# Kernel optimization log

Hardware: AMD Instinct MI355X
Metric: run time of the kernel (lower is better)

The kernel has to match this reference:

```python
import jax, jax.numpy as jnp
from jax import lax
import numpy as np

LOGZERO = -1e10  # matches the repo's `logzero` sentinel


def setup_inputs() -> dict:
    key = jax.random.key(0)
    k1, k2, k3, k4 = jax.random.split(key, 4)
    bs, xmax, vocab, ymax = 32, 1024, 1000, 128
    # CTC log-probabilities (ctc_generator output is log_softmax in the repo)
    ctc_out = jax.nn.log_softmax(
        jax.random.normal(k1, (bs, xmax, vocab), jnp.float32), axis=-1)
    src_size = jax.random.randint(k2, (bs,), xmax // 2, xmax + 1)
    src_mask = (jnp.arange(xmax)[None, :] < src_size[:, None])[:, None, :]  # [bs,1,xmax] bool
    ys = jax.random.randint(k3, (bs, ymax), 1, vocab)   # non-blank labels
    ylens = jax.random.randint(k4, (bs,), ymax // 2, ymax + 1)
    return {"ctc_out": ctc_out, "src_mask": src_mask, "src_size": src_size,
            "ys": ys, "ylens": ylens, "blank": 0}


def reference(ctc_out, src_mask, src_size, ys, ylens, blank):
    bs, xmax, vocab = ctc_out.shape
    ymax = ys.shape[1]
    L = 2 * ymax + 1  # blank-interleaved path length

    # mask invalid frames to logzero (masked_fill in torch)
    lp = jnp.where(src_mask.transpose(0, 2, 1), ctc_out, LOGZERO)  # [bs,xmax,vocab]

    # blank-interleaved path: [blank, y1, blank, y2, ..., blank]
    path = jnp.full((bs, L), blank, dtype=ys.dtype).at[:, 1::2].set(ys)
    path_lens = 2 * ylens + 1

    # log-probs gathered along the path: [xmax, bs, L] (time-major for scan)
    lp_path = jnp.take_along_axis(
        lp, jnp.broadcast_to(path[:, None, :], (bs, xmax, L)), axis=2)
    lp_path = lp_path.transpose(1, 0, 2)

    same_tr = path[:, :-2] == path[:, 2:]                 # [bs, L-2]
    idx = jnp.arange(L)
    outside = idx[None, :] >= path_lens[:, None]          # [bs, L]

    alpha0 = jnp.full((bs, L), LOGZERO, jnp.float32).at[:, 0].set(0.0)

    def step(alpha, lp_t):
        m0 = alpha
        m1 = jnp.concatenate([jnp.full((bs, 1), LOGZERO, alpha.dtype), alpha[:, :-1]], axis=1)
        m2 = jnp.concatenate([jnp.full((bs, 2), LOGZERO, alpha.dtype),
                              jnp.where(same_tr, LOGZERO, alpha[:, :-2])], axis=1)
        mat = jnp.stack([m0, m1, m2])                     # [3, bs, L]
        max_prob = jnp.max(mat, axis=0)
        arg = jnp.argmax(mat, axis=0)
        bp_t = idx[None, :] - arg                          # back-pointer (path position)
        max_prob = jnp.where(outside, LOGZERO, max_prob)
        alpha_new = max_prob + lp_t
        return alpha_new, (alpha_new, bp_t)

    _, (alpha_hist, bp) = lax.scan(step, alpha0, lp_path)  # [xmax,bs,L] each
    alpha_full = jnp.concatenate([alpha0[None], alpha_hist], axis=0)  # [xmax+1,bs,L]

    b_idx = jnp.arange(bs)
    alpha_at = alpha_full[src_size, b_idx]                 # [bs, L] alpha at t = src_size
    s1 = alpha_at[b_idx, path_lens - 1]
    s2 = alpha_at[b_idx, path_lens - 2]
    start = jnp.where(s1 > s2, path_lens - 1, path_lens - 2)
    score = jnp.maximum(s1, s2)                            # best alignment log-prob per utt

    # vectorized backtrace over all batches (reverse scan over time)
    def back_step(carry, t):
        tt = jnp.minimum(t + 1, xmax - 1)
        prev = bp[tt, b_idx, carry]                        # bp[b, t+1, state_{t+1}]
        val = jnp.where(t == src_size - 1, start,
                        jnp.where(t < src_size - 1, prev, 0))
        return val, val

    ts = jnp.arange(xmax - 1, -1, -1)
    _, states_rev = lax.scan(back_step, jnp.zeros((bs,), start.dtype), ts)
    states = states_rev[::-1].T                            # [bs, xmax] path positions

    aligned = jnp.take_along_axis(path, states, axis=1)    # [bs, xmax] tokens
    shift = jnp.concatenate([jnp.zeros((bs, 1), aligned.dtype), aligned[:, :-1]], axis=1)
    aligned = jnp.where(aligned == shift, 0, aligned)      # collapse repeats to 0
    shift2 = jnp.concatenate([jnp.zeros((bs, 1), aligned.dtype), aligned[:, :-1]], axis=1)

    csum = jnp.cumsum((shift2 != blank).astype(jnp.int32), axis=1)  # [bs, xmax]
    tm = csum[:, None, :] == jnp.arange(ymax + 1)[None, :, None]    # [bs, ymax+1, xmax]
    last = tm[:, -1, :] & src_mask[:, 0, :]
    last = last.at[b_idx, src_size - 1].set(True)
    tm = tm.at[:, -1, :].set(last)
    trigger_mask = tm & src_mask                           # & x_mask from FaNat.forward

    return score, trigger_mask, ylens + 1
```

## Files before the change

### kernel.cpp

```cpp
#include <hip/hip_runtime.h>
#include <stdint.h>

#define LOGZERO (-1e10f)

static constexpr int BS    = 32;
static constexpr int XMAX  = 1024;
static constexpr int VOCAB = 1000;
static constexpr int YMAX  = 128;
static constexpr int NROWS = YMAX + 1;
static constexpr int CH    = 8;
static constexpr int NPROD = 8;
static constexpr int NWAVES = 1 + NPROD;
static constexpr int NPAIR = XMAX / 2;
static constexpr size_t LPWS_BYTES = (size_t)BS * XMAX * 256 * 4;

__device__ __forceinline__ float rot1(float x) {
    int r = __builtin_amdgcn_update_dpp(0, __float_as_int(x),
                                        0x13C , 0xF, 0xF, false);
    return __int_as_float(r);
}

__global__ __launch_bounds__(256) void k_gather(
    const float* __restrict__ ctc, const int* __restrict__ src_size,
    const int* __restrict__ ys, const int* __restrict__ blankp,
    float* __restrict__ lp_ws)
{
    const int blk  = blockIdx.x;
    const int b    = blk >> 4;
    const int seg  = blk & 15;
    const int wid  = threadIdx.x >> 6;
    const int lane = threadIdx.x & 63;
    const int ss   = src_size[b];
    const int bv   = blankp[0];
    const int tokA = ys[b * YMAX + 2 * lane];
    const int tokB = ys[b * YMAX + 2 * lane + 1];
    const float* baseg = ctc + (size_t)b * XMAX * VOCAB;
    float* basew = lp_ws + (size_t)b * XMAX * 256 + lane * 4;
    const int t0 = seg * 64 + wid * 16;
    #pragma unroll 4
    for (int r = 0; r < 16; ++r) {
        const int t = t0 + r;
        if (t < ss) {
            const float* rp = baseg + (size_t)t * VOCAB;
            float vb = rp[bv], va = rp[tokA], vc = rp[tokB];
            *reinterpret_cast<float4*>(basew + (size_t)t * 256) =
                make_float4(vb, va, vb, vc);
        }
    }
}

#define VSTEP(qq, PK, SHIFT, RBIT) do {                                     \
    float rot = rot1(a3);                       \
    float p3  = (lane == 0) ? LZ : rot;                                     \
    float sk1 = al1 ? p3 : LZ;                                              \
    float sk3 = al3 ? a1 : LZ;                                              \
    float m0 = fmaxf(a0, p3);                                               \
    float m1 = fmaxf(fmaxf(a1, a0), sk1);                                   \
    float m2 = fmaxf(a2, a1);                                               \
    float m3 = fmaxf(fmaxf(a3, a2), sk3);                                   \
    unsigned gb = (a0 == m0 ? 0u : 1u)                                      \
                | (a1 == m1 ? 0u : (a0 == m1 ? 4u : 8u))                    \
                | (a2 == m2 ? 0u : 16u)                                     \
                | (a3 == m3 ? 0u : (a2 == m3 ? 64u : 128u));                \
    if (W4) {                                                               \
        float m4 = fmaxf(a4, rot);                                          \
        g4acc |= (a4 == m4 ? 0u : 1u) << (RBIT);                            \
        a4 = m4 + (qq).x;                       \
    }                                                                       \
    a0 = m0 + (qq).x; a1 = m1 + (qq).y; a2 = m2 + (qq).z; a3 = m3 + (qq).w; \
    PK |= gb << (SHIFT);                                                    \
} while (0)

template<bool W4>
__device__ __forceinline__ void viterbi_loop(
    int lane, int ss, bool al1, bool al3, float LZ,
    float (&buf)[2][CH][256], unsigned int* bpb32, unsigned char* g4pack,
    float& a0, float& a1, float& a2, float& a3, float& a4)
{
    const int nfull = ss >> 3;
    const int mrem  = ss & 7;
    for (int c = 0; c < nfull; ++c) {
        __builtin_amdgcn_s_barrier();
        asm volatile("" ::: "memory");
        __builtin_amdgcn_sched_barrier(0);
        const int cb = c & 1;
        float4 q[CH];
        #pragma unroll
        for (int r = 0; r < CH; ++r)
            q[r] = *reinterpret_cast<const float4*>(&buf[cb][r][lane * 4]);
        unsigned int pkA = 0, pkB = 0, g4acc = 0;
        #pragma unroll
        for (int r = 0; r < 4; ++r) VSTEP(q[r], pkA, r * 8, r);
        #pragma unroll
        for (int r = 4; r < 8; ++r) VSTEP(q[r], pkB, (r - 4) * 8, r);
        bpb32[(2 * c) * 64 + lane]     = pkA;
        bpb32[(2 * c + 1) * 64 + lane] = pkB;
        if (W4) { if (lane == 0) g4pack[c] = (unsigned char)g4acc; }
    }
    if (mrem) {
        __builtin_amdgcn_s_barrier();
        asm volatile("" ::: "memory");
        __builtin_amdgcn_sched_barrier(0);
        const int cb = nfull & 1;
        float4 q[CH];
        #pragma unroll
        for (int r = 0; r < CH; ++r)
            q[r] = *reinterpret_cast<const float4*>(&buf[cb][r][lane * 4]);
        unsigned int pkA = 0, pkB = 0, g4acc = 0;
        #pragma unroll
        for (int r = 0; r < 4; ++r)
            if (r < mrem) VSTEP(q[r], pkA, r * 8, r);
        #pragma unroll
        for (int r = 4; r < 8; ++r)
            if (r < mrem) VSTEP(q[r], pkB, (r - 4) * 8, r);
        bpb32[(2 * nfull) * 64 + lane] = pkA;
        if (mrem > 4) bpb32[(2 * nfull + 1) * 64 + lane] = pkB;
        if (W4) { if (lane == 0) g4pack[nfull] = (unsigned char)g4acc; }
    }
}

template<bool STAGED>
__global__ __launch_bounds__(64 * NWAVES) void k_viterbi(
    const float* __restrict__ ctc, const float* __restrict__ lp_ws,
    const int* __restrict__ src_size,
    const int* __restrict__ ys, const int* __restrict__ ylens,
    const int* __restrict__ blankp, int* __restrict__ csum_ws,
    float* __restrict__ out)
{
    __shared__ float buf[2][CH][256];
    __shared__ unsigned int  bpb32[(XMAX / 4) * 64];
    __shared__ unsigned char  g4pack[XMAX / CH];
    __shared__ unsigned short bp2[NPAIR * 64];
    __shared__ unsigned char  bp2_256[NPAIR];
    __shared__ unsigned short st_lds[XMAX];
    __shared__ int ysl[YMAX];

    const int b    = blockIdx.x;
    const int tid  = threadIdx.x;
    const int wid  = tid >> 6;
    const int lane = tid & 63;
    const int ss   = src_size[b];
    const int yl   = ylens[b];
    const int bv   = blankp[0];
    const int plen = 2 * yl + 1;
    const float LZ = LOGZERO;

    for (int j = tid; j < YMAX; j += 64 * NWAVES) ysl[j] = ys[b * YMAX + j];
    for (int t = tid; t < XMAX; t += 64 * NWAVES) st_lds[t] = 0;
    __syncthreads();

    const int nchunk = (ss + CH - 1) / CH;
    const float* baseg = ctc + (size_t)b * XMAX * VOCAB;

    int start = 0;

    if (wid == 0) {
        const int tokA = ysl[2 * lane];
        const int tokB = ysl[2 * lane + 1];
        const bool al1 = (lane > 0) && (tokA != ysl[2 * lane - 1]);
        const bool al3 = (tokB != tokA);

        float a0 = (lane == 0) ? 0.0f : LZ;
        float a1 = LZ, a2 = LZ, a3 = LZ, a4 = LZ;

        if (plen > 256)
            viterbi_loop<true >(lane, ss, al1, al3, LZ, buf, bpb32, g4pack,
                                a0, a1, a2, a3, a4);
        else
            viterbi_loop<false>(lane, ss, al1, al3, LZ, buf, bpb32, g4pack,
                                a0, a1, a2, a3, a4);

        auto getA = [&](int idx) -> float {
            if (idx == 256) return __shfl(a4, 0);
            int k = idx & 3;
            float pick = (k == 0) ? a0 : (k == 1) ? a1 : (k == 2) ? a2 : a3;
            return __shfl(pick, idx >> 2);
        };
        const float s1v = getA(plen - 1), s2v = getA(plen - 2);
        const float score = (s1v > s2v) ? s1v : s2v;
        start = (s1v > s2v) ? (plen - 1) : (plen - 2);
        if (lane == 0) {
            out[b] = score;
            out[32 + (size_t)BS * NROWS * XMAX + b] = (float)(yl + 1);
        }
    } else if (STAGED) {
        const int pr = wid - 1;
        const float* basew = lp_ws + (size_t)b * XMAX * 256 + lane * 4;
        auto ldrow = [&](int cc) -> float4 {
            int tn = cc * CH + pr; if (tn > XMAX - 1) tn = XMAX - 1;
            return *reinterpret_cast<const float4*>(basew + (size_t)tn * 256);
        };
        float4 v0 = ldrow(0), v1 = ldrow(1), v2 = ldrow(2), v3 = ldrow(3);
        int c = 0;
        for (;;) {
            *reinterpret_cast<float4*>(&buf[c & 1][pr][lane * 4]) = v0;
            v0 = ldrow(c + 4);
            asm volatile("s_waitcnt lgkmcnt(0)" ::: "memory");
            __builtin_amdgcn_s_barrier();
            if (++c >= nchunk) break;
            *reinterpret_cast<float4*>(&buf[c & 1][pr][lane * 4]) = v1;
            v1 = ldrow(c + 4);
            asm volatile("s_waitcnt lgkmcnt(0)" ::: "memory");
            __builtin_amdgcn_s_barrier();
            if (++c >= nchunk) break;
            *reinterpret_cast<float4*>(&buf[c & 1][pr][lane * 4]) = v2;
            v2 = ldrow(c + 4);
            asm volatile("s_waitcnt lgkmcnt(0)" ::: "memory");
            __builtin_amdgcn_s_barrier();
            if (++c >= nchunk) break;
            *reinterpret_cast<float4*>(&buf[c & 1][pr][lane * 4]) = v3;
            v3 = ldrow(c + 4);
            asm volatile("s_waitcnt lgkmcnt(0)" ::: "memory");
            __builtin_amdgcn_s_barrier();
            if (++c >= nchunk) break;
        }
    } else {
        const int pr = wid - 1;
        const int tokA = ysl[2 * lane];
        const int tokB = ysl[2 * lane + 1];
        int t0 = pr; if (t0 >= ss) t0 = ss - 1;
        const float* r0 = baseg + (size_t)t0 * VOCAB;
        float vb0 = r0[bv], va0 = r0[tokA], vc0 = r0[tokB];
        int t1 = CH + pr; if (t1 >= ss) t1 = ss - 1;
        const float* r1 = baseg + (size_t)t1 * VOCAB;
        float vb1 = r1[bv], va1 = r1[tokA], vc1 = r1[tokB];
        for (int c = 0; c < nchunk; ++c) {
            if (c & 1) {
                *reinterpret_cast<float4*>(&buf[1][pr][lane * 4]) =
                    make_float4(vb1, va1, vb1, vc1);
                int tn = (c + 2) * CH + pr; if (tn >= ss) tn = ss - 1;
                const float* r = baseg + (size_t)tn * VOCAB;
                vb1 = r[bv]; va1 = r[tokA]; vc1 = r[tokB];
            } else {
                *reinterpret_cast<float4*>(&buf[0][pr][lane * 4]) =
                    make_float4(vb0, va0, vb0, vc0);
                int tn = (c + 2) * CH + pr; if (tn >= ss) tn = ss - 1;
                const float* r = baseg + (size_t)tn * VOCAB;
                vb0 = r[bv]; va0 = r[tokA]; vc0 = r[tokB];
            }
            asm volatile("s_waitcnt lgkmcnt(0)" ::: "memory");
            __builtin_amdgcn_s_barrier();
        }
    }
    __syncthreads();

    const unsigned char* bpb8 = reinterpret_cast<const unsigned char*>(bpb32);
    #define BPBYTE(t, l) ((int)bpb8[(((t) >> 2) * 64 + (l)) * 4 + ((t) & 3)])

    const int pmax = (ss - 1) >> 1;
    for (int p = 1 + wid; p <= pmax; p += NWAVES) {
        int oOdd  = BPBYTE(2 * p + 1, lane);
        int oEven = BPBYTE(2 * p, lane);
        int uEven = (lane > 0) ? BPBYTE(2 * p, lane - 1) : 0;
        int evenWin = uEven | (oEven << 8);
        unsigned int acc = 0;
        #pragma unroll
        for (int k = 0; k < 4; ++k) {
            int a1v = (oOdd >> (2 * k)) & 3;
            int sh  = 2 * k - 2 * a1v + 8;
            int a2v = (evenWin >> sh) & 3;
            acc |= (unsigned)(a1v | (a2v << 2)) << (4 * k);
        }
        bp2[p * 64 + lane] = (unsigned short)acc;
        const int tOdd = 2 * p + 1, tEven = 2 * p;
        int a16 = (g4pack[tOdd >> 3] >> (tOdd & 7)) & 1;
        int a26 = (a16 == 0) ? ((g4pack[tEven >> 3] >> (tEven & 7)) & 1)
                             : ((BPBYTE(tEven, 63) >> 6) & 3);
        if (lane == 0) bp2_256[p] = (unsigned char)(a16 | (a26 << 2));
    }
    __syncthreads();

    if (tid == 0) {
        int s = start, tc = ss - 1;
        st_lds[tc] = (unsigned short)s;
        if ((tc & 1) == 0 && tc >= 1) {
            int arg;
            if (s == 256) arg = (g4pack[tc >> 3] >> (tc & 7)) & 1;
            else arg = (BPBYTE(tc, s >> 2) >> ((s & 3) * 2)) & 3;
            s -= arg; --tc; st_lds[tc] = (unsigned short)s;
        }
        while (tc > 1) {
            int n;
            if (s == 256) n = bp2_256[tc >> 1];
            else n = (bp2[(tc >> 1) * 64 + (s >> 2)] >> ((s & 3) * 4)) & 0xF;
            int sA = s - (n & 3);
            int sB = sA - (n >> 2);
            st_lds[tc - 1] = (unsigned short)sA;
            st_lds[tc - 2] = (unsigned short)sB;
            s = sB; tc -= 2;
        }
        if (tc == 1) {
            int arg;
            if (s == 256) arg = (g4pack[0] >> 1) & 1;
            else arg = (BPBYTE(1, s >> 2) >> ((s & 3) * 2)) & 3;
            s -= arg; st_lds[0] = (unsigned short)s;
        }
    }
    #undef BPBYTE
    __syncthreads();

    if (wid == 0) {
        auto tok_lds = [&](int stv) -> int { return (stv & 1) ? ysl[stv >> 1] : bv; };
        const int t0c = lane * 16;
        int prev_raw = (t0c == 0) ? 0 : tok_lds(st_lds[t0c - 1]);
        int cnt = 0;
        int csl[16];
        #pragma unroll
        for (int i = 0; i < 16; ++i) {
            int raw = tok_lds(st_lds[t0c + i]);
            int ac = (raw == prev_raw) ? 0 : raw;
            prev_raw = raw;
            csl[i] = cnt;
            cnt += (ac != bv) ? 1 : 0;
        }
        int v = cnt;
        #pragma unroll
        for (int off = 1; off < 64; off <<= 1) {
            int u = __shfl_up(v, off);
            if (lane >= off) v += u;
        }
        const int base_c = v - cnt;
        int* co = csum_ws + b * XMAX + t0c;
        #pragma unroll
        for (int i = 0; i < 16; ++i) co[i] = base_c + csl[i];
    }
}

__global__ __launch_bounds__(256) void k_mask(
    const int* __restrict__ csum_ws, const int* __restrict__ src_size,
    float* __restrict__ out)
{
    int bj = blockIdx.x;
    int b = bj / NROWS, j = bj - b * NROWS;
    int ss = src_size[b];
    const int* cs = csum_ws + b * XMAX;
    float* orow = out + 32 + (size_t)bj * XMAX;
    int t = threadIdx.x * 4;
    float4 v;
    float* vp = &v.x;
    #pragma unroll
    for (int i = 0; i < 4; ++i) {
        int tt = t + i;
        int c = cs[tt];
        bool in = tt < ss;
        bool val;
        if (j < YMAX) val = (c == j) && in;
        else          val = ((c == YMAX) || (tt == ss - 1)) && in;
        vp[i] = val ? 1.0f : 0.0f;
    }
    *(float4*)(orow + t) = v;
}

extern "C" void kernel_launch(void* const* d_in, const int* in_sizes, int n_in,
                              void* d_out, int out_size, void* d_ws, size_t ws_size,
                              hipStream_t stream) {
    const float* ctc      = (const float*)d_in[0];
    const int*   src_size = (const int*)d_in[2];
    const int*   ys       = (const int*)d_in[3];
    const int*   ylens    = (const int*)d_in[4];
    const int*   blankp   = (const int*)d_in[5];
    float* out = (float*)d_out;

    const size_t need = LPWS_BYTES + (size_t)BS * XMAX * sizeof(int);
    if (ws_size >= need) {
        float* lp_ws   = (float*)d_ws;
        int*   csum_ws = (int*)((char*)d_ws + LPWS_BYTES);
        k_gather<<<BS * 16, 256, 0, stream>>>(ctc, src_size, ys, blankp, lp_ws);
        k_viterbi<true><<<BS, 64 * NWAVES, 0, stream>>>(
            ctc, lp_ws, src_size, ys, ylens, blankp, csum_ws, out);
        k_mask<<<BS * NROWS, 256, 0, stream>>>(csum_ws, src_size, out);
    } else {
        int* csum_ws = (int*)d_ws;
        k_viterbi<false><<<BS, 64 * NWAVES, 0, stream>>>(
            ctc, nullptr, src_size, ys, ylens, blankp, csum_ws, out);
        k_mask<<<BS * NROWS, 256, 0, stream>>>(csum_ws, src_size, out);
    }
}
```

Before: 340.3 us.

## Stream staged log-probs into LDS via direct global-to-LDS loads in Viterbi wave

In the staged path, the Viterbi wave now fetches its own chunks from the gathered workspace using global_load_lds, which writes straight into a triple-buffered LDS ring. This replaces the eight producer waves and their per-chunk block barriers. Synchronisation drops to vmcnt/lgkmcnt waits inside one wave, removing barrier latency from the serial recurrence. The cost is a larger LDS buffer and reliance on the async-load counter accounting, with three chunks kept in flight. The producer waves still launch but sit idle in the staged path.

```diff
diff --git a/kernel.cpp b/kernel.cpp
--- a/kernel.cpp
+++ b/kernel.cpp
@@ -18,6 +18,12 @@
     int r = __builtin_amdgcn_update_dpp(0, __float_as_int(x),
                                         0x13C , 0xF, 0xF, false);
     return __int_as_float(r);
+}
+
+__device__ __forceinline__ void gload16(const float* g, float* l) {
+    __builtin_amdgcn_global_load_lds(
+        (const __attribute__((address_space(1))) void*)g,
+        (__attribute__((address_space(3))) void*)l, 16, 0, 0);
 }
 
 __global__ __launch_bounds__(256) void k_gather(
@@ -72,9 +78,70 @@
 } while (0)
 
 template<bool W4>
-__device__ __forceinline__ void viterbi_loop(
+__device__ __forceinline__ void viterbi_loop_staged(
     int lane, int ss, bool al1, bool al3, float LZ,
-    float (&buf)[2][CH][256], unsigned int* bpb32, unsigned char* g4pack,
+    float (&buf)[3][CH][256], unsigned int* bpb32, unsigned char* g4pack,
+    const float* basew,
+    float& a0, float& a1, float& a2, float& a3, float& a4)
+{
+    const int nfull = ss >> 3;
+    const int mrem  = ss & 7;
+
+    auto issue_chunk = [&](int cc, int cb) {
+        int ccl = cc; if (ccl > XMAX / CH - 1) ccl = XMAX / CH - 1;
+        const float* g0 = basew + (size_t)ccl * (CH * 256);
+        #pragma unroll
+        for (int r = 0; r < CH; ++r)
+            gload16(g0 + r * 256, &buf[cb][r][0]);
+    };
+    issue_chunk(0, 0); issue_chunk(1, 1); issue_chunk(2, 2);
+
+    int cb = 0;
+    for (int c = 0; c < nfull; ++c) {
+        asm volatile("s_waitcnt vmcnt(16)" ::: "memory");
+        __builtin_amdgcn_sched_barrier(0);
+        float4 q[CH];
+        #pragma unroll
+        for (int r = 0; r < CH; ++r)
+            q[r] = *reinterpret_cast<const float4*>(&buf[cb][r][lane * 4]);
+        asm volatile("s_waitcnt lgkmcnt(0)" ::: "memory");
+        __builtin_amdgcn_sched_barrier(0);
+        issue_chunk(c + 3, cb);
+        __builtin_amdgcn_sched_barrier(0);
+        unsigned int pkA = 0, pkB = 0, g4acc = 0;
+        #pragma unroll
+        for (int r = 0; r < 4; ++r) VSTEP(q[r], pkA, r * 8, r);
+        #pragma unroll
+        for (int r = 4; r < 8; ++r) VSTEP(q[r], pkB, (r - 4) * 8, r);
+        bpb32[(2 * c) * 64 + lane]     = pkA;
+        bpb32[(2 * c + 1) * 64 + lane] = pkB;
+        if (W4) { if (lane == 0) g4pack[c] = (unsigned char)g4acc; }
+        cb = (cb == 2) ? 0 : cb + 1;
+    }
+    if (mrem) {
+        asm volatile("s_waitcnt vmcnt(16)" ::: "memory");
+        __builtin_amdgcn_sched_barrier(0);
+        float4 q[CH];
+        #pragma unroll
+        for (int r = 0; r < CH; ++r)
+            q[r] = *reinterpret_cast<const float4*>(&buf[cb][r][lane * 4]);
+        unsigned int pkA = 0, pkB = 0, g4acc = 0;
+        #pragma unroll
+        for (int r = 0; r < 4; ++r)
+            if (r < mrem) VSTEP(q[r], pkA, r * 8, r);
+        #pragma unroll
+        for (int r = 4; r < 8; ++r)
+            if (r < mrem) VSTEP(q[r], pkB, (r - 4) * 8, r);
+        bpb32[(2 * nfull) * 64 + lane] = pkA;
+        if (mrem > 4) bpb32[(2 * nfull + 1) * 64 + lane] = pkB;
+        if (W4) { if (lane == 0) g4pack[nfull] = (unsigned char)g4acc; }
+    }
+}
+
+template<bool W4>
+__device__ __forceinline__ void viterbi_loop_ring(
+    int lane, int ss, bool al1, bool al3, float LZ,
+    float (&buf)[3][CH][256], unsigned int* bpb32, unsigned char* g4pack,
     float& a0, float& a1, float& a2, float& a3, float& a4)
 {
     const int nfull = ss >> 3;
@@ -127,7 +194,7 @@
     const int* __restrict__ blankp, int* __restrict__ csum_ws,
     float* __restrict__ out)
 {
-    __shared__ float buf[2][CH][256];
+    __shared__ float buf[3][CH][256];
     __shared__ unsigned int  bpb32[(XMAX / 4) * 64];
     __shared__ unsigned char  g4pack[XMAX / CH];
     __shared__ unsigned short bp2[NPAIR * 64];
@@ -163,12 +230,22 @@
         float a0 = (lane == 0) ? 0.0f : LZ;
         float a1 = LZ, a2 = LZ, a3 = LZ, a4 = LZ;
 
-        if (plen > 256)
-            viterbi_loop<true >(lane, ss, al1, al3, LZ, buf, bpb32, g4pack,
-                                a0, a1, a2, a3, a4);
-        else
-            viterbi_loop<false>(lane, ss, al1, al3, LZ, buf, bpb32, g4pack,
-                                a0, a1, a2, a3, a4);
+        if (STAGED) {
+            const float* basew = lp_ws + (size_t)b * XMAX * 256 + lane * 4;
+            if (plen > 256)
+                viterbi_loop_staged<true >(lane, ss, al1, al3, LZ, buf, bpb32,
+                                           g4pack, basew, a0, a1, a2, a3, a4);
+            else
+                viterbi_loop_staged<false>(lane, ss, al1, al3, LZ, buf, bpb32,
+                                           g4pack, basew, a0, a1, a2, a3, a4);
+        } else {
+            if (plen > 256)
+                viterbi_loop_ring<true >(lane, ss, al1, al3, LZ, buf, bpb32,
+                                         g4pack, a0, a1, a2, a3, a4);
+            else
+                viterbi_loop_ring<false>(lane, ss, al1, al3, LZ, buf, bpb32,
+                                         g4pack, a0, a1, a2, a3, a4);
+        }
 
         auto getA = [&](int idx) -> float {
             if (idx == 256) return __shfl(a4, 0);
@@ -183,38 +260,7 @@
             out[b] = score;
             out[32 + (size_t)BS * NROWS * XMAX + b] = (float)(yl + 1);
         }
-    } else if (STAGED) {
-        const int pr = wid - 1;
-        const float* basew = lp_ws + (size_t)b * XMAX * 256 + lane * 4;
-        auto ldrow = [&](int cc) -> float4 {
-            int tn = cc * CH + pr; if (tn > XMAX - 1) tn = XMAX - 1;
-            return *reinterpret_cast<const float4*>(basew + (size_t)tn * 256);
-        };
-        float4 v0 = ldrow(0), v1 = ldrow(1), v2 = ldrow(2), v3 = ldrow(3);
-        int c = 0;
-        for (;;) {
-            *reinterpret_cast<float4*>(&buf[c & 1][pr][lane * 4]) = v0;
-            v0 = ldrow(c + 4);
-            asm volatile("s_waitcnt lgkmcnt(0)" ::: "memory");
-            __builtin_amdgcn_s_barrier();
-            if (++c >= nchunk) break;
-            *reinterpret_cast<float4*>(&buf[c & 1][pr][lane * 4]) = v1;
-            v1 = ldrow(c + 4);
-            asm volatile("s_waitcnt lgkmcnt(0)" ::: "memory");
-            __builtin_amdgcn_s_barrier();
-            if (++c >= nchunk) break;
-            *reinterpret_cast<float4*>(&buf[c & 1][pr][lane * 4]) = v2;
-            v2 = ldrow(c + 4);
-            asm volatile("s_waitcnt lgkmcnt(0)" ::: "memory");
-            __builtin_amdgcn_s_barrier();
-            if (++c >= nchunk) break;
-            *reinterpret_cast<float4*>(&buf[c & 1][pr][lane * 4]) = v3;
-            v3 = ldrow(c + 4);
-            asm volatile("s_waitcnt lgkmcnt(0)" ::: "memory");
-            __builtin_amdgcn_s_barrier();
-            if (++c >= nchunk) break;
-        }
-    } else {
+    } else if (!STAGED) {
         const int pr = wid - 1;
         const int tokA = ysl[2 * lane];
         const int tokB = ysl[2 * lane + 1];
```

Measured after the change: 349.1 us. +2.6%, slower.

## Fuse gather, Viterbi and mask into one kernel with per-segment flag sync

Applied to the files above, without the earlier changes.

Merges the separate gather, Viterbi and mask kernels into one launch. Extra blocks gather the path log-probs into the workspace and publish per-segment release flags. The Viterbi producer waves spin on those flags so decoding can begin before the whole gather finishes. The cumsum and trigger-mask output are also computed inside the Viterbi block, which drops the csum workspace round trip and two launches. The cost is a memset plus spin-wait synchronisation, which relies on the Viterbi blocks (lowest IDs) being scheduled alongside the gather blocks, and the mask writes now come from only 32 blocks.

```diff
diff --git a/kernel.cpp b/kernel.cpp
--- a/kernel.cpp
+++ b/kernel.cpp
@@ -12,41 +12,14 @@
 static constexpr int NPROD = 8;
 static constexpr int NWAVES = 1 + NPROD;
 static constexpr int NPAIR = XMAX / 2;
+static constexpr int NSEG  = 16;
 static constexpr size_t LPWS_BYTES = (size_t)BS * XMAX * 256 * 4;
+static constexpr size_t FLAGS_BYTES = (size_t)BS * NSEG * sizeof(int);
 
 __device__ __forceinline__ float rot1(float x) {
     int r = __builtin_amdgcn_update_dpp(0, __float_as_int(x),
                                         0x13C , 0xF, 0xF, false);
     return __int_as_float(r);
-}
-
-__global__ __launch_bounds__(256) void k_gather(
-    const float* __restrict__ ctc, const int* __restrict__ src_size,
-    const int* __restrict__ ys, const int* __restrict__ blankp,
-    float* __restrict__ lp_ws)
-{
-    const int blk  = blockIdx.x;
-    const int b    = blk >> 4;
-    const int seg  = blk & 15;
-    const int wid  = threadIdx.x >> 6;
-    const int lane = threadIdx.x & 63;
-    const int ss   = src_size[b];
-    const int bv   = blankp[0];
-    const int tokA = ys[b * YMAX + 2 * lane];
-    const int tokB = ys[b * YMAX + 2 * lane + 1];
-    const float* baseg = ctc + (size_t)b * XMAX * VOCAB;
-    float* basew = lp_ws + (size_t)b * XMAX * 256 + lane * 4;
-    const int t0 = seg * 64 + wid * 16;
-    #pragma unroll 4
-    for (int r = 0; r < 16; ++r) {
-        const int t = t0 + r;
-        if (t < ss) {
-            const float* rp = baseg + (size_t)t * VOCAB;
-            float vb = rp[bv], va = rp[tokA], vc = rp[tokB];
-            *reinterpret_cast<float4*>(basew + (size_t)t * 256) =
-                make_float4(vb, va, vb, vc);
-        }
-    }
 }
 
 #define VSTEP(qq, PK, SHIFT, RBIT) do {                                     \
@@ -72,7 +45,7 @@
 } while (0)
 
 template<bool W4>
-__device__ __forceinline__ void viterbi_loop(
+__device__ __forceinline__ void viterbi_loop_ring(
     int lane, int ss, bool al1, bool al3, float LZ,
     float (&buf)[2][CH][256], unsigned int* bpb32, unsigned char* g4pack,
     float& a0, float& a1, float& a2, float& a3, float& a4)
@@ -119,13 +92,11 @@
     }
 }
 
-template<bool STAGED>
-__global__ __launch_bounds__(64 * NWAVES) void k_viterbi(
-    const float* __restrict__ ctc, const float* __restrict__ lp_ws,
-    const int* __restrict__ src_size,
+__global__ __launch_bounds__(64 * NWAVES) void k_fused(
+    const float* __restrict__ ctc, float* __restrict__ lp_ws,
+    int* __restrict__ flags, const int* __restrict__ src_size,
     const int* __restrict__ ys, const int* __restrict__ ylens,
-    const int* __restrict__ blankp, int* __restrict__ csum_ws,
-    float* __restrict__ out)
+    const int* __restrict__ blankp, float* __restrict__ out)
 {
     __shared__ float buf[2][CH][256];
     __shared__ unsigned int  bpb32[(XMAX / 4) * 64];
@@ -133,12 +104,42 @@
     __shared__ unsigned short bp2[NPAIR * 64];
     __shared__ unsigned char  bp2_256[NPAIR];
     __shared__ unsigned short st_lds[XMAX];
+    __shared__ int cs_lds[XMAX];
     __shared__ int ysl[YMAX];
 
-    const int b    = blockIdx.x;
     const int tid  = threadIdx.x;
     const int wid  = tid >> 6;
     const int lane = tid & 63;
+
+    if (blockIdx.x >= BS) {
+        const int gidx = blockIdx.x - BS;
+        const int seg  = gidx >> 5;
+        const int b    = gidx & 31;
+        const int ss   = src_size[b];
+        const int bv   = blankp[0];
+        const int tokA = ys[b * YMAX + 2 * lane];
+        const int tokB = ys[b * YMAX + 2 * lane + 1];
+        const float* baseg = ctc + (size_t)b * XMAX * VOCAB;
+        float* basew = lp_ws + (size_t)b * XMAX * 256 + lane * 4;
+        for (int r = wid; r < 64; r += NWAVES) {
+            const int t = seg * 64 + r;
+            if (t < ss) {
+                const float* rp = baseg + (size_t)t * VOCAB;
+                float vb = rp[bv], va = rp[tokA], vc = rp[tokB];
+                *reinterpret_cast<float4*>(basew + (size_t)t * 256) =
+                    make_float4(vb, va, vb, vc);
+            }
+        }
+        __syncthreads();
+        if (tid == 0) {
+            __threadfence();
+            __hip_atomic_store(&flags[b * NSEG + seg], 1,
+                               __ATOMIC_RELEASE, __HIP_MEMORY_SCOPE_AGENT);
+        }
+        return;
+    }
+
+    const int b    = blockIdx.x;
     const int ss   = src_size[b];
     const int yl   = ylens[b];
     const int bv   = blankp[0];
@@ -150,8 +151,6 @@
     __syncthreads();
 
     const int nchunk = (ss + CH - 1) / CH;
-    const float* baseg = ctc + (size_t)b * XMAX * VOCAB;
-
     int start = 0;
 
     if (wid == 0) {
@@ -164,11 +163,11 @@
         float a1 = LZ, a2 = LZ, a3 = LZ, a4 = LZ;
 
         if (plen > 256)
-            viterbi_loop<true >(lane, ss, al1, al3, LZ, buf, bpb32, g4pack,
-                                a0, a1, a2, a3, a4);
+            viterbi_loop_ring<true >(lane, ss, al1, al3, LZ, buf, bpb32,
+                                     g4pack, a0, a1, a2, a3, a4);
         else
-            viterbi_loop<false>(lane, ss, al1, al3, LZ, buf, bpb32, g4pack,
-                                a0, a1, a2, a3, a4);
+            viterbi_loop_ring<false>(lane, ss, al1, al3, LZ, buf, bpb32,
+                                     g4pack, a0, a1, a2, a3, a4);
 
         auto getA = [&](int idx) -> float {
             if (idx == 256) return __shfl(a4, 0);
@@ -183,36 +182,198 @@
             out[b] = score;
             out[32 + (size_t)BS * NROWS * XMAX + b] = (float)(yl + 1);
         }
-    } else if (STAGED) {
+    } else {
         const int pr = wid - 1;
         const float* basew = lp_ws + (size_t)b * XMAX * 256 + lane * 4;
+        int* flg = flags + b * NSEG;
+        auto waitseg = [&](int s) {
+            while (__hip_atomic_load(&flg[s], __ATOMIC_ACQUIRE,
+                                     __HIP_MEMORY_SCOPE_AGENT) == 0)
+                __builtin_amdgcn_s_sleep(2);
+        };
         auto ldrow = [&](int cc) -> float4 {
             int tn = cc * CH + pr; if (tn > XMAX - 1) tn = XMAX - 1;
             return *reinterpret_cast<const float4*>(basew + (size_t)tn * 256);
         };
+        waitseg(0);
         float4 v0 = ldrow(0), v1 = ldrow(1), v2 = ldrow(2), v3 = ldrow(3);
+        int slast = 0;
         int c = 0;
-        for (;;) {
-            *reinterpret_cast<float4*>(&buf[c & 1][pr][lane * 4]) = v0;
-            v0 = ldrow(c + 4);
-            asm volatile("s_waitcnt lgkmcnt(0)" ::: "memory");
-            __builtin_amdgcn_s_barrier();
-            if (++c >= nchunk) break;
-            *reinterpret_cast<float4*>(&buf[c & 1][pr][lane * 4]) = v1;
-            v1 = ldrow(c + 4);
-            asm volatile("s_waitcnt lgkmcnt(0)" ::: "memory");
-            __builtin_amdgcn_s_barrier();
-            if (++c >= nchunk) break;
-            *reinterpret_cast<float4*>(&buf[c & 1][pr][lane * 4]) = v2;
-            v2 = ldrow(c + 4);
-            asm volatile("s_waitcnt lgkmcnt(0)" ::: "memory");
-            __builtin_amdgcn_s_barrier();
-            if (++c >= nchunk) break;
-            *reinterpret_cast<float4*>(&buf[c & 1][pr][lane * 4]) = v3;
-            v3 = ldrow(c + 4);
-            asm volatile("s_waitcnt lgkmcnt(0)" ::: "memory");
-            __builtin_amdgcn_s_barrier();
-            if (++c >= nchunk) break;
+#define PPHASE(VV)                                                          \
+        *reinterpret_cast<float4*>(&buf[c & 1][pr][lane * 4]) = VV;         \
+        { int row = (c + 4) * CH + pr; if (row > XMAX - 1) row = XMAX - 1;  \
+          int sn = row >> 6;                                                \
+          if (sn != slast) { waitseg(sn); slast = sn; } }                   \
+        VV = ldrow(c + 4);                                                  \
+        asm volatile("s_waitcnt lgkmcnt(0)" ::: "memory");                  \
+        __builtin_amdgcn_s_barrier();                                       \
+        if (++c >= nchunk) break;
+        for (;;) { PPHASE(v0) PPHASE(v1) PPHASE(v2) PPHASE(v3) }
+#undef PPHASE
+    }
+    __syncthreads();
+
+    const unsigned char* bpb8 = reinterpret_cast<const unsigned char*>(bpb32);
+    #define BPBYTE(t, l) ((int)bpb8[(((t) >> 2) * 64 + (l)) * 4 + ((t) & 3)])
+
+    const int pmax = (ss - 1) >> 1;
+    for (int p = 1 + wid; p <= pmax; p += NWAVES) {
+        int oOdd  = BPBYTE(2 * p + 1, lane);
+        int oEven = BPBYTE(2 * p, lane);
+        int uEven = (lane > 0) ? BPBYTE(2 * p, lane - 1) : 0;
+        int evenWin = uEven | (oEven << 8);
+        unsigned int acc = 0;
+        #pragma unroll
+        for (int k = 0; k < 4; ++k) {
+            int a1v = (oOdd >> (2 * k)) & 3;
+            int sh  = 2 * k - 2 * a1v + 8;
+            int a2v = (evenWin >> sh) & 3;
+            acc |= (unsigned)(a1v | (a2v << 2)) << (4 * k);
+        }
+        bp2[p * 64 + lane] = (unsigned short)acc;
+        const int tOdd = 2 * p + 1, tEven = 2 * p;
+        int a16 = (g4pack[tOdd >> 3] >> (tOdd & 7)) & 1;
+        int a26 = (a16 == 0) ? ((g4pack[tEven >> 3] >> (tEven & 7)) & 1)
+                             : ((BPBYTE(tEven, 63) >> 6) & 3);
+        if (lane == 0) bp2_256[p] = (unsigned char)(a16 | (a26 << 2));
+    }
+    __syncthreads();
+
+    if (tid == 0) {
+        int s = start, tc = ss - 1;
+        st_lds[tc] = (unsigned short)s;
+        if ((tc & 1) == 0 && tc >= 1) {
+            int arg;
+            if (s == 256) arg = (g4pack[tc >> 3] >> (tc & 7)) & 1;
+            else arg = (BPBYTE(tc, s >> 2) >> ((s & 3) * 2)) & 3;
+            s -= arg; --tc; st_lds[tc] = (unsigned short)s;
+        }
+        while (tc > 1) {
+            int n;
+            if (s == 256) n = bp2_256[tc >> 1];
+            else n = (bp2[(tc >> 1) * 64 + (s >> 2)] >> ((s & 3) * 4)) & 0xF;
+            int sA = s - (n & 3);
+            int sB = sA - (n >> 2);
+            st_lds[tc - 1] = (unsigned short)sA;
+            st_lds[tc - 2] = (unsigned short)sB;
+            s = sB; tc -= 2;
+        }
+        if (tc == 1) {
+            int arg;
+            if (s == 256) arg = (g4pack[0] >> 1) & 1;
+            else arg = (BPBYTE(1, s >> 2) >> ((s & 3) * 2)) & 3;
+            s -= arg; st_lds[0] = (unsigned short)s;
+        }
+    }
+    #undef BPBYTE
+    __syncthreads();
+
+    if (wid == 0) {
+        auto tok_lds = [&](int stv) -> int { return (stv & 1) ? ysl[stv >> 1] : bv; };
+        const int t0c = lane * 16;
+        int prev_raw = (t0c == 0) ? 0 : tok_lds(st_lds[t0c - 1]);
+        int cnt = 0;
+        int csl[16];
+        #pragma unroll
+        for (int i = 0; i < 16; ++i) {
+            int raw = tok_lds(st_lds[t0c + i]);
+            int ac = (raw == prev_raw) ? 0 : raw;
+            prev_raw = raw;
+            csl[i] = cnt;
+            cnt += (ac != bv) ? 1 : 0;
+        }
+        int v = cnt;
+        #pragma unroll
+        for (int off = 1; off < 64; off <<= 1) {
+            int u = __shfl_up(v, off);
+            if (lane >= off) v += u;
+        }
+        const int base_c = v - cnt;
+        #pragma unroll
+        for (int i = 0; i < 16; ++i) cs_lds[t0c + i] = base_c + csl[i];
+    }
+    __syncthreads();
+
+    for (int j = wid; j < NROWS; j += NWAVES) {
+        float* orow = out + 32 + ((size_t)b * NROWS + j) * XMAX;
+        const int t0c = lane * 16;
+        #pragma unroll
+        for (int q4 = 0; q4 < 4; ++q4) {
+            const int t = t0c + q4 * 4;
+            float4 v;
+            float* vp = &v.x;
+            #pragma unroll
+            for (int i = 0; i < 4; ++i) {
+                int tt = t + i;
+                int c = cs_lds[tt];
+                bool in = tt < ss;
+                bool val;
+                if (j < YMAX) val = (c == j) && in;
+                else          val = ((c == YMAX) || (tt == ss - 1)) && in;
+                vp[i] = val ? 1.0f : 0.0f;
+            }
+            *(float4*)(orow + t) = v;
+        }
+    }
+}
+
+__global__ __launch_bounds__(64 * NWAVES) void k_viterbi_fb(
+    const float* __restrict__ ctc, const int* __restrict__ src_size,
+    const int* __restrict__ ys, const int* __restrict__ ylens,
+    const int* __restrict__ blankp, int* __restrict__ csum_ws,
+    float* __restrict__ out)
+{
+    __shared__ float buf[2][CH][256];
+    __shared__ unsigned int  bpb32[(XMAX / 4) * 64];
+    __shared__ unsigned char  g4pack[XMAX / CH];
+    __shared__ unsigned short bp2[NPAIR * 64];
+    __shared__ unsigned char  bp2_256[NPAIR];
+    __shared__ unsigned short st_lds[XMAX];
+    __shared__ int ysl[YMAX];
+
+    const int b    = blockIdx.x;
+    const int tid  = threadIdx.x;
+    const int wid  = tid >> 6;
+    const int lane = tid & 63;
+    const int ss   = src_size[b];
+    const int yl   = ylens[b];
+    const int bv   = blankp[0];
+    const int plen = 2 * yl + 1;
+    const float LZ = LOGZERO;
+
+    for (int j = tid; j < YMAX; j += 64 * NWAVES) ysl[j] = ys[b * YMAX + j];
+    for (int t = tid; t < XMAX; t += 64 * NWAVES) st_lds[t] = 0;
+    __syncthreads();
+
+    const int nchunk = (ss + CH - 1) / CH;
+    const float* baseg = ctc + (size_t)b * XMAX * VOCAB;
+    int start = 0;
+
+    if (wid == 0) {
+        const int tokA = ysl[2 * lane];
+        const int tokB = ysl[2 * lane + 1];
+        const bool al1 = (lane > 0) && (tokA != ysl[2 * lane - 1]);
+        const bool al3 = (tokB != tokA);
+        float a0 = (lane == 0) ? 0.0f : LZ;
+        float a1 = LZ, a2 = LZ, a3 = LZ, a4 = LZ;
+        if (plen > 256)
+            viterbi_loop_ring<true >(lane, ss, al1, al3, LZ, buf, bpb32,
+                                     g4pack, a0, a1, a2, a3, a4);
+        else
+            viterbi_loop_ring<false>(lane, ss, al1, al3, LZ, buf, bpb32,
+                                     g4pack, a0, a1, a2, a3, a4);
+        auto getA = [&](int idx) -> float {
+            if (idx == 256) return __shfl(a4, 0);
+            int k = idx & 3;
+            float pick = (k == 0) ? a0 : (k == 1) ? a1 : (k == 2) ? a2 : a3;
+            return __shfl(pick, idx >> 2);
+        };
+        const float s1v = getA(plen - 1), s2v = getA(plen - 2);
+        const float score = (s1v > s2v) ? s1v : s2v;
+        start = (s1v > s2v) ? (plen - 1) : (plen - 2);
+        if (lane == 0) {
+            out[b] = score;
+            out[32 + (size_t)BS * NROWS * XMAX + b] = (float)(yl + 1);
         }
     } else {
         const int pr = wid - 1;
@@ -246,7 +407,6 @@
 
     const unsigned char* bpb8 = reinterpret_cast<const unsigned char*>(bpb32);
     #define BPBYTE(t, l) ((int)bpb8[(((t) >> 2) * 64 + (l)) * 4 + ((t) & 3)])
-
     const int pmax = (ss - 1) >> 1;
     for (int p = 1 + wid; p <= pmax; p += NWAVES) {
         int oOdd  = BPBYTE(2 * p + 1, lane);
@@ -361,18 +521,17 @@
     const int*   blankp   = (const int*)d_in[5];
     float* out = (float*)d_out;
 
-    const size_t need = LPWS_BYTES + (size_t)BS * XMAX * sizeof(int);
+    const size_t need = LPWS_BYTES + FLAGS_BYTES;
     if (ws_size >= need) {
-        float* lp_ws   = (float*)d_ws;
-        int*   csum_ws = (int*)((char*)d_ws + LPWS_BYTES);
-        k_gather<<<BS * 16, 256, 0, stream>>>(ctc, src_size, ys, blankp, lp_ws);
-        k_viterbi<true><<<BS, 64 * NWAVES, 0, stream>>>(
-            ctc, lp_ws, src_size, ys, ylens, blankp, csum_ws, out);
-        k_mask<<<BS * NROWS, 256, 0, stream>>>(csum_ws, src_size, out);
+        float* lp_ws = (float*)d_ws;
+        int*   flags = (int*)((char*)d_ws + LPWS_BYTES);
+        hipMemsetAsync(flags, 0, FLAGS_BYTES, stream);
+        k_fused<<<BS + BS * NSEG, 64 * NWAVES, 0, stream>>>(
+            ctc, lp_ws, flags, src_size, ys, ylens, blankp, out);
     } else {
         int* csum_ws = (int*)d_ws;
-        k_viterbi<false><<<BS, 64 * NWAVES, 0, stream>>>(
-            ctc, nullptr, src_size, ys, ylens, blankp, csum_ws, out);
+        k_viterbi_fb<<<BS, 64 * NWAVES, 0, stream>>>(
+            ctc, src_size, ys, ylens, blankp, csum_ws, out);
         k_mask<<<BS * NROWS, 256, 0, stream>>>(csum_ws, src_size, out);
     }
 }
```

Result: slower. 380.1 us (+11.7%).
